# Kernel optimization log

Measured on AMD Instinct MI355X. Metric: run time of the kernel, lower is better.

## Reference

```python
import jax, jax.numpy as jnp
import numpy as np

B, S, D, H = 2, 2048, 1024, 16
HD = D // H  # 64

def setup_inputs() -> dict:
    key = jax.random.key(0)
    ks = jax.random.split(key, 11)
    s = 1.0 / np.sqrt(D)
    inp = {
        "q": jax.random.normal(ks[0], (B, S, D), jnp.float32),
        "k": jax.random.normal(ks[1], (B, S, D), jnp.float32),
        "v": jax.random.normal(ks[2], (B, S, D), jnp.float32),
        "Wq": jax.random.normal(ks[3], (D, D), jnp.float32) * s,
        "bq": jnp.zeros((D,), jnp.float32),
        "Wk": jax.random.normal(ks[4], (D, D), jnp.float32) * s,
        "bk": jnp.zeros((D,), jnp.float32),
        "Wv": jax.random.normal(ks[5], (D, D), jnp.float32) * s,
        "bv": jnp.zeros((D,), jnp.float32),
        "Wo": jax.random.normal(ks[6], (D, D), jnp.float32) * s,
        "bo": jnp.zeros((D,), jnp.float32),
    }
    return inp

def _split_heads(x):
    # [B,S,D] -> [B,H,S,HD]
    b = x.shape[0]
    return x.reshape(b, -1, H, HD).transpose(0, 2, 1, 3)

def reference(q, k, v, Wq, bq, Wk, bk, Wv, bv, Wo, bo):
    qh = _split_heads(q @ Wq.T + bq)
    kh = _split_heads(k @ Wk.T + bk)
    vh = _split_heads(v @ Wv.T + bv)
    scale = 1.0 / jnp.sqrt(jnp.asarray(HD, qh.dtype))
    scores = jnp.einsum("bhqd,bhkd->bhqk", qh, kh) * scale  # [B,H,S,S]
    atten = jax.nn.softmax(scores, axis=-1)  # dropout is eval-mode no-op
    ctx = jnp.einsum("bhqk,bhkd->bhqd", atten, vh)
    out = ctx.transpose(0, 2, 1, 3).reshape(q.shape[0], -1, D)
    return out @ Wo.T + bo, atten
```

## Files before the change

kernel.cpp:

```cpp
#include <hip/hip_runtime.h>
#include <cstdint>

#define B_ 2
#define S_ 2048
#define D_ 1024
#define H_ 16

typedef __bf16 bf16x8 __attribute__((ext_vector_type(8)));
typedef float  f32x4  __attribute__((ext_vector_type(4)));

__device__ __forceinline__ void g2l16(const void* g, void* l) {
  auto* gp = reinterpret_cast<const __attribute__((address_space(1))) uint32_t*>(
      reinterpret_cast<uintptr_t>(g));
  auto* lp = reinterpret_cast<__attribute__((address_space(3))) uint32_t*>(
      reinterpret_cast<uintptr_t>(l));
  __builtin_amdgcn_global_load_lds(gp, lp, 16, 0, 0);
}

__device__ __forceinline__ float exp2_hw(float x) {
#if __has_builtin(__builtin_amdgcn_exp2f)
  return __builtin_amdgcn_exp2f(x);
#else
  return __exp2f(x);
#endif
}

struct CvtArgs {
  const float* s[7];
  __bf16* d[7];
  int n[7];
};

__global__ __launch_bounds__(256) void k_cvt(CvtArgs a) {
  int t = blockIdx.y;
  long i = (long)blockIdx.x * blockDim.x + threadIdx.x;
  long base = i * 8;
  if (base >= a.n[t]) return;
  const float4* sp = (const float4*)(a.s[t] + base);
  float4 x = sp[0], y = sp[1];
  bf16x8 o;
  o[0] = (__bf16)x.x; o[1] = (__bf16)x.y; o[2] = (__bf16)x.z; o[3] = (__bf16)x.w;
  o[4] = (__bf16)y.x; o[5] = (__bf16)y.y; o[6] = (__bf16)y.z; o[7] = (__bf16)y.w;
  *(bf16x8*)(a.d[t] + base) = o;
}

__global__ __launch_bounds__(256, 3) void k_proj(
    const __bf16* __restrict__ Xq, const __bf16* __restrict__ Xk, const __bf16* __restrict__ Xv,
    const __bf16* __restrict__ Wq, const __bf16* __restrict__ Wk, const __bf16* __restrict__ Wv,
    const float* __restrict__ bq, const float* __restrict__ bk, const float* __restrict__ bv,
    __bf16* __restrict__ Oq, __bf16* __restrict__ Ok, __bf16* __restrict__ Ov)
{
  int z = blockIdx.z;
  const __bf16* X = (z == 0) ? Xq : (z == 1) ? Xk : Xv;
  const __bf16* W = (z == 0) ? Wq : (z == 1) ? Wk : Wv;
  const float* bias = (z == 0) ? bq : (z == 1) ? bk : bv;
  __bf16* O = (z == 0) ? Oq : (z == 1) ? Ok : Ov;
  float scale = (z == 0) ? 0.180336880111183f : 1.0f;

  __shared__ bf16x8 As[3][512];
  __shared__ bf16x8 Bs[3][512];

  int t = threadIdx.x, lane = t & 63, w = t >> 6;
  int l15 = lane & 15, l4 = lane >> 4;
  int wr = w >> 1, wc = w & 1;
  int m0 = blockIdx.y * 128, n0 = blockIdx.x * 128;

  int srow = t >> 2, sc = t & 3;
  int ldsoff = __builtin_amdgcn_readfirstlane(w * 1024);
  const __bf16* Xs = X + (size_t)(m0 + srow) * 1024 + sc * 8;
  const __bf16* Wsp = W + (size_t)(n0 + srow) * 1024 + sc * 8;

#define PSTAGE(buf, kt)                                                        \
  {                                                                            \
    _Pragma("unroll")                                                          \
    for (int i = 0; i < 2; ++i) {                                              \
      int lo = __builtin_amdgcn_readfirstlane(i * 4096 + ldsoff);              \
      g2l16(Xs + (size_t)i * 64 * 1024 + (kt) * 32, (char*)As[buf] + lo);      \
      g2l16(Wsp + (size_t)i * 64 * 1024 + (kt) * 32, (char*)Bs[buf] + lo);     \
    }                                                                          \
  }

  f32x4 acc[4][4] = {};

  PSTAGE(0, 0)
  PSTAGE(1, 1)
  asm volatile("s_waitcnt vmcnt(4)" ::: "memory");
  __builtin_amdgcn_s_barrier();
  __builtin_amdgcn_sched_barrier(0);

  int ring = 0;
  for (int kt = 0; kt < 32; ++kt) {
    int cur = ring;
    int rp2 = (ring == 0) ? 2 : ring - 1;
    if (kt + 2 < 32) PSTAGE(rp2, kt + 2)
    __builtin_amdgcn_sched_barrier(0);

    bf16x8 af[4], bfr[4];
#pragma unroll
    for (int i = 0; i < 4; ++i) af[i] = As[cur][(wr * 64 + i * 16 + l15) * 4 + l4];
#pragma unroll
    for (int j = 0; j < 4; ++j) bfr[j] = Bs[cur][(wc * 64 + j * 16 + l15) * 4 + l4];
#pragma unroll
    for (int i = 0; i < 4; ++i)
#pragma unroll
      for (int j = 0; j < 4; ++j)
        acc[i][j] = __builtin_amdgcn_mfma_f32_16x16x32_bf16(af[i], bfr[j], acc[i][j], 0, 0, 0);

    if (kt < 30) {
      asm volatile("s_waitcnt vmcnt(4)" ::: "memory");
      __builtin_amdgcn_s_barrier();
      __builtin_amdgcn_sched_barrier(0);
    } else if (kt == 30) {
      asm volatile("s_waitcnt vmcnt(0)" ::: "memory");
      __builtin_amdgcn_s_barrier();
      __builtin_amdgcn_sched_barrier(0);
    }
    ring = (ring == 2) ? 0 : ring + 1;
  }
#undef PSTAGE

#pragma unroll
  for (int j = 0; j < 4; ++j) {
    int col = n0 + wc * 64 + j * 16 + l15;
    float bv_ = bias[col];
    int h = col >> 6, hd = col & 63;
#pragma unroll
    for (int i = 0; i < 4; ++i) {
#pragma unroll
      for (int r = 0; r < 4; ++r) {
        int row = m0 + wr * 64 + i * 16 + l4 * 4 + r;
        int b = row >> 11, ss = row & 2047;
        float val = (acc[i][j][r] + bv_) * scale;
        O[(((size_t)b * H_ + h) * S_ + ss) * 64 + hd] = (__bf16)val;
      }
    }
  }
}

__global__ __launch_bounds__(256) void k_trans(const __bf16* __restrict__ Vh,
                                               __bf16* __restrict__ VhT)
{
  __shared__ __bf16 Tt[64][72];
  int bid = blockIdx.x;
  int bh = bid >> 5, st = bid & 31;
  int t = threadIdx.x;
  int sr = t >> 2, dc = (t & 3) * 16;
  const __bf16* src = Vh + (((size_t)bh * S_) + st * 64 + sr) * 64 + dc;
  *(bf16x8*)&Tt[sr][dc] = *(const bf16x8*)src;
  *(bf16x8*)&Tt[sr][dc + 8] = *(const bf16x8*)(src + 8);
  __syncthreads();
  int dr = t >> 2, s0 = (t & 3) * 16;
  bf16x8 o0, o1;
#pragma unroll
  for (int ii = 0; ii < 8; ++ii) { o0[ii] = Tt[s0 + ii][dr]; o1[ii] = Tt[s0 + 8 + ii][dr]; }
  __bf16* dst = VhT + ((size_t)bh * 64 + dr) * S_ + st * 64 + s0;
  *(bf16x8*)dst = o0;
  *(bf16x8*)(dst + 8) = o1;
}

__global__ __launch_bounds__(512, 4) void k_attn(
    const __bf16* __restrict__ Qh, const __bf16* __restrict__ Kh,
    const __bf16* __restrict__ VhT, float* __restrict__ atten,
    __bf16* __restrict__ ctxb)
{
  __shared__ bf16x8 KVl[3][1024];
  __shared__ bf16x8 Pl[8 * 176];

  int bid = blockIdx.x;
  int sb = (bid & 7) * 64 + (bid >> 3);
  int bh = sb >> 4, qt = sb & 15;
  int t = threadIdx.x, lane = t & 63, w = t >> 6;
  int l15 = lane & 15, l4 = lane >> 4;
  int q0 = qt * 128 + w * 16;

  const __bf16* Qp = Qh + ((size_t)bh * S_ + q0) * 64;
  bf16x8 qf0 = *(const bf16x8*)(Qp + (size_t)l15 * 64 + l4 * 8);
  bf16x8 qf1 = *(const bf16x8*)(Qp + (size_t)l15 * 64 + 32 + l4 * 8);

  int srow = t >> 3, sc8 = t & 7;
  int scs = sc8 ^ (srow & 7);
  int wbase = __builtin_amdgcn_readfirstlane(w * 1024);

  const __bf16* KpS = Kh + (size_t)bh * S_ * 64 + (size_t)srow * 64 + scs * 8;
  const __bf16* VpS = VhT + (size_t)bh * 64 * S_ + (size_t)srow * S_ + scs * 8;

  float l_part[4] = {0.f, 0.f, 0.f, 0.f};

#define ASTAGE(buf, kt)                                                        \
  {                                                                            \
    g2l16(KpS + (size_t)(kt) * 8192, (char*)KVl[buf] + wbase);                 \
    g2l16(KpS + (size_t)(kt) * 8192 + 4096, (char*)KVl[buf] + 8192 + wbase);   \
  }

  ASTAGE(0, 0)
  ASTAGE(1, 1)
  asm volatile("s_waitcnt vmcnt(2)" ::: "memory");
  __builtin_amdgcn_s_barrier();
  __builtin_amdgcn_sched_barrier(0);

  {
    int ring = 0;
    for (int kt = 0; kt < 16; ++kt) {
      int cur = ring;
      int rp2 = (ring == 0) ? 2 : ring - 1;
      if (kt + 2 < 16) ASTAGE(rp2, kt + 2)
      __builtin_amdgcn_sched_barrier(0);

#pragma unroll
      for (int t8 = 0; t8 < 8; ++t8) {
        int kr = t8 * 16 + l15;
        bf16x8 kf0 = KVl[cur][kr * 8 + ((l4) ^ (kr & 7))];
        bf16x8 kf1 = KVl[cur][kr * 8 + ((4 + l4) ^ (kr & 7))];
        f32x4 a_ = {0.f, 0.f, 0.f, 0.f};
        a_ = __builtin_amdgcn_mfma_f32_16x16x32_bf16(qf0, kf0, a_, 0, 0, 0);
        a_ = __builtin_amdgcn_mfma_f32_16x16x32_bf16(qf1, kf1, a_, 0, 0, 0);
#pragma unroll
        for (int r = 0; r < 4; ++r) l_part[r] += exp2_hw(a_[r]);
      }

      if (kt < 14) {
        asm volatile("s_waitcnt vmcnt(2)" ::: "memory");
        __builtin_amdgcn_s_barrier();
        __builtin_amdgcn_sched_barrier(0);
      } else if (kt == 14) {
        asm volatile("s_waitcnt vmcnt(0)" ::: "memory");
        __builtin_amdgcn_s_barrier();
        __builtin_amdgcn_sched_barrier(0);
      }
      ring = (ring == 2) ? 0 : ring + 1;
    }
  }
#undef ASTAGE

  float inv_l[4];
#pragma unroll
  for (int r = 0; r < 4; ++r) {
    float l = l_part[r];
    l += __shfl_xor(l, 1);
    l += __shfl_xor(l, 2);
    l += __shfl_xor(l, 4);
    l += __shfl_xor(l, 8);
    inv_l[r] = 1.0f / l;
  }

  __builtin_amdgcn_s_barrier();
  __builtin_amdgcn_sched_barrier(0);

  f32x4 ctx[4] = {};
  float* aRow = atten + ((size_t)bh * S_ + q0) * S_;
  __bf16* PlW = (__bf16*)(Pl + w * 176);

#define BSTAGE(buf, kt)                                                        \
  {                                                                            \
    g2l16(KpS + (size_t)(kt) * 4096, (char*)KVl[buf] + wbase);                 \
    g2l16(VpS + (size_t)(kt) * 64, (char*)KVl[buf] + 8192 + wbase);            \
  }

  BSTAGE(0, 0)
  BSTAGE(1, 1)
  asm volatile("s_waitcnt vmcnt(2)" ::: "memory");
  __builtin_amdgcn_s_barrier();
  __builtin_amdgcn_sched_barrier(0);

  {
    int ring = 0;
    for (int kt = 0; kt < 32; ++kt) {
      int cur = ring;
      int rp2 = (ring == 0) ? 2 : ring - 1;
      if (kt + 2 < 32) BSTAGE(rp2, kt + 2)
      __builtin_amdgcn_sched_barrier(0);

      f32x4 sc[4];
#pragma unroll
      for (int t8 = 0; t8 < 4; ++t8) {
        int kr = t8 * 16 + l15;
        bf16x8 kf0 = KVl[cur][kr * 8 + ((l4) ^ (kr & 7))];
        bf16x8 kf1 = KVl[cur][kr * 8 + ((4 + l4) ^ (kr & 7))];
        f32x4 a_ = {0.f, 0.f, 0.f, 0.f};
        a_ = __builtin_amdgcn_mfma_f32_16x16x32_bf16(qf0, kf0, a_, 0, 0, 0);
        a_ = __builtin_amdgcn_mfma_f32_16x16x32_bf16(qf1, kf1, a_, 0, 0, 0);
        sc[t8] = a_;
      }

#pragma unroll
      for (int t8 = 0; t8 < 4; ++t8) {
#pragma unroll
        for (int r = 0; r < 4; ++r) {
          float p = exp2_hw(sc[t8][r]) * inv_l[r];
          aRow[(size_t)(l4 * 4 + r) * S_ + kt * 64 + t8 * 16 + l15] = p;
          PlW[(l4 * 4 + r) * 88 + t8 * 16 + l15] = (__bf16)p;
        }
      }

#pragma unroll
      for (int kc = 0; kc < 2; ++kc) {
        bf16x8 pa = Pl[w * 176 + l15 * 11 + kc * 4 + l4];
#pragma unroll
        for (int dt = 0; dt < 4; ++dt) {
          int vr = dt * 16 + l15;
          bf16x8 vf = KVl[cur][512 + vr * 8 + ((kc * 4 + l4) ^ (vr & 7))];
          ctx[dt] = __builtin_amdgcn_mfma_f32_16x16x32_bf16(pa, vf, ctx[dt], 0, 0, 0);
        }
      }

      if (kt < 31) {
        asm volatile("s_waitcnt vmcnt(18)" ::: "memory");
        __builtin_amdgcn_s_barrier();
        __builtin_amdgcn_sched_barrier(0);
      }
      ring = (ring == 2) ? 0 : ring + 1;
    }
  }
#undef BSTAGE

  int b = bh >> 4, h = bh & 15;
#pragma unroll
  for (int dt = 0; dt < 4; ++dt) {
#pragma unroll
    for (int r = 0; r < 4; ++r) {
      size_t row = (size_t)b * S_ + q0 + l4 * 4 + r;
      ctxb[row * D_ + h * 64 + dt * 16 + l15] = (__bf16)ctx[dt][r];
    }
  }
}

__global__ __launch_bounds__(256, 3) void k_out(
    const __bf16* __restrict__ X, const __bf16* __restrict__ W,
    const float* __restrict__ bias, float* __restrict__ O)
{
  __shared__ bf16x8 As[3][512];
  __shared__ bf16x8 Bs[3][512];

  int t = threadIdx.x, lane = t & 63, w = t >> 6;
  int l15 = lane & 15, l4 = lane >> 4;
  int wr = w >> 1, wc = w & 1;
  int m0 = blockIdx.y * 128, n0 = blockIdx.x * 128;

  int srow = t >> 2, sc = t & 3;
  int ldsoff = __builtin_amdgcn_readfirstlane(w * 1024);
  const __bf16* Xs = X + (size_t)(m0 + srow) * 1024 + sc * 8;
  const __bf16* Wsp = W + (size_t)(n0 + srow) * 1024 + sc * 8;

#define PSTAGE(buf, kt)                                                        \
  {                                                                            \
    _Pragma("unroll")                                                          \
    for (int i = 0; i < 2; ++i) {                                              \
      int lo = __builtin_amdgcn_readfirstlane(i * 4096 + ldsoff);              \
      g2l16(Xs + (size_t)i * 64 * 1024 + (kt) * 32, (char*)As[buf] + lo);      \
      g2l16(Wsp + (size_t)i * 64 * 1024 + (kt) * 32, (char*)Bs[buf] + lo);     \
    }                                                                          \
  }

  f32x4 acc[4][4] = {};

  PSTAGE(0, 0)
  PSTAGE(1, 1)
  asm volatile("s_waitcnt vmcnt(4)" ::: "memory");
  __builtin_amdgcn_s_barrier();
  __builtin_amdgcn_sched_barrier(0);

  int ring = 0;
  for (int kt = 0; kt < 32; ++kt) {
    int cur = ring;
    int rp2 = (ring == 0) ? 2 : ring - 1;
    if (kt + 2 < 32) PSTAGE(rp2, kt + 2)
    __builtin_amdgcn_sched_barrier(0);

    bf16x8 af[4], bfr[4];
#pragma unroll
    for (int i = 0; i < 4; ++i) af[i] = As[cur][(wr * 64 + i * 16 + l15) * 4 + l4];
#pragma unroll
    for (int j = 0; j < 4; ++j) bfr[j] = Bs[cur][(wc * 64 + j * 16 + l15) * 4 + l4];
#pragma unroll
    for (int i = 0; i < 4; ++i)
#pragma unroll
      for (int j = 0; j < 4; ++j)
        acc[i][j] = __builtin_amdgcn_mfma_f32_16x16x32_bf16(af[i], bfr[j], acc[i][j], 0, 0, 0);

    if (kt < 30) {
      asm volatile("s_waitcnt vmcnt(4)" ::: "memory");
      __builtin_amdgcn_s_barrier();
      __builtin_amdgcn_sched_barrier(0);
    } else if (kt == 30) {
      asm volatile("s_waitcnt vmcnt(0)" ::: "memory");
      __builtin_amdgcn_s_barrier();
      __builtin_amdgcn_sched_barrier(0);
    }
    ring = (ring == 2) ? 0 : ring + 1;
  }
#undef PSTAGE

#pragma unroll
  for (int j = 0; j < 4; ++j) {
    int col = n0 + wc * 64 + j * 16 + l15;
    float bv_ = bias[col];
#pragma unroll
    for (int i = 0; i < 4; ++i) {
#pragma unroll
      for (int r = 0; r < 4; ++r) {
        int row = m0 + wr * 64 + i * 16 + l4 * 4 + r;
        O[(size_t)row * 1024 + col] = acc[i][j][r] + bv_;
      }
    }
  }
}

extern "C" void kernel_launch(void* const* d_in, const int* in_sizes, int n_in,
                              void* d_out, int out_size, void* d_ws, size_t ws_size,
                              hipStream_t stream)
{
  const float* q  = (const float*)d_in[0];
  const float* k  = (const float*)d_in[1];
  const float* v  = (const float*)d_in[2];
  const float* Wq = (const float*)d_in[3];
  const float* bq = (const float*)d_in[4];
  const float* Wk = (const float*)d_in[5];
  const float* bk = (const float*)d_in[6];
  const float* Wv = (const float*)d_in[7];
  const float* bv = (const float*)d_in[8];
  const float* Wo = (const float*)d_in[9];
  const float* bo = (const float*)d_in[10];

  const size_t NBSD = (size_t)B_ * S_ * D_;
  const size_t NDD  = (size_t)D_ * D_;

  float* out = (float*)d_out;
  float* atten = out + NBSD;

  if (ws_size < 2 * (NBSD * 4 + NDD * 4 + NBSD * 4)) return;

  __bf16* ws = (__bf16*)d_ws;
  __bf16* qb  = ws;
  __bf16* kb  = ws + NBSD;
  __bf16* vb  = ws + 2 * NBSD;
  __bf16* Wqb = ws + 3 * NBSD;
  __bf16* Wkb = Wqb + NDD;
  __bf16* Wvb = Wkb + NDD;
  __bf16* Wob = Wvb + NDD;
  __bf16* Qh  = Wob + NDD;
  __bf16* Kh  = Qh + NBSD;
  __bf16* Vh  = Kh + NBSD;
  __bf16* VhT = Vh + NBSD;
  __bf16* ctxb = qb;

  CvtArgs ca;
  ca.s[0] = q;  ca.d[0] = qb;  ca.n[0] = (int)NBSD;
  ca.s[1] = k;  ca.d[1] = kb;  ca.n[1] = (int)NBSD;
  ca.s[2] = v;  ca.d[2] = vb;  ca.n[2] = (int)NBSD;
  ca.s[3] = Wq; ca.d[3] = Wqb; ca.n[3] = (int)NDD;
  ca.s[4] = Wk; ca.d[4] = Wkb; ca.n[4] = (int)NDD;
  ca.s[5] = Wv; ca.d[5] = Wvb; ca.n[5] = (int)NDD;
  ca.s[6] = Wo; ca.d[6] = Wob; ca.n[6] = (int)NDD;

  k_cvt<<<dim3(2048, 7), 256, 0, stream>>>(ca);
  k_proj<<<dim3(8, 32, 3), 256, 0, stream>>>(qb, kb, vb, Wqb, Wkb, Wvb,
                                             bq, bk, bv, Qh, Kh, Vh);
  k_trans<<<dim3(1024), 256, 0, stream>>>(Vh, VhT);
  k_attn<<<dim3(512), 512, 0, stream>>>(Qh, Kh, VhT, atten, ctxb);
  k_out<<<dim3(8, 32), 256, 0, stream>>>(ctxb, Wob, bo, out);
}
```

Baseline: 261.5 us.

## Fuse activation fp32→bf16 conversion and V transpose into projection GEMM

The projection kernel now loads fp32 activations directly into registers, converts them to bf16 and writes them to LDS, so the separate conversion pass over q/k/v is dropped and k_cvt only converts weights. The V projection epilogue stages its tile through LDS and writes the transposed layout directly, which removes the k_trans kernel and its extra global round trip. The cost is that A-tile loads become register-staged with double buffering instead of async global-to-LDS copies, and the GEMM main loop now reads twice the bytes for the activation operand.

New measurement: 256.6 us. Within noise of the previous version (-1.8%).

```diff
diff --git a/kernel.cpp b/kernel.cpp
--- a/kernel.cpp
+++ b/kernel.cpp
@@ -7,6 +7,7 @@
 #define H_ 16
 
 typedef __bf16 bf16x8 __attribute__((ext_vector_type(8)));
+typedef __bf16 bf16x4 __attribute__((ext_vector_type(4)));
 typedef float  f32x4  __attribute__((ext_vector_type(4)));
 
 __device__ __forceinline__ void g2l16(const void* g, void* l) {
@@ -26,16 +27,13 @@
 }
 
 struct CvtArgs {
-  const float* s[7];
-  __bf16* d[7];
-  int n[7];
+  const float* s[4];
+  __bf16* d[4];
 };
 
 __global__ __launch_bounds__(256) void k_cvt(CvtArgs a) {
   int t = blockIdx.y;
-  long i = (long)blockIdx.x * blockDim.x + threadIdx.x;
-  long base = i * 8;
-  if (base >= a.n[t]) return;
+  long base = ((long)blockIdx.x * blockDim.x + threadIdx.x) * 8;
   const float4* sp = (const float4*)(a.s[t] + base);
   float4 x = sp[0], y = sp[1];
   bf16x8 o;
@@ -45,117 +43,161 @@
 }
 
 __global__ __launch_bounds__(256, 3) void k_proj(
-    const __bf16* __restrict__ Xq, const __bf16* __restrict__ Xk, const __bf16* __restrict__ Xv,
+    const float* __restrict__ Xq, const float* __restrict__ Xk, const float* __restrict__ Xv,
     const __bf16* __restrict__ Wq, const __bf16* __restrict__ Wk, const __bf16* __restrict__ Wv,
     const float* __restrict__ bq, const float* __restrict__ bk, const float* __restrict__ bv,
-    __bf16* __restrict__ Oq, __bf16* __restrict__ Ok, __bf16* __restrict__ Ov)
+    __bf16* __restrict__ Oq, __bf16* __restrict__ Ok, __bf16* __restrict__ OvT)
 {
   int z = blockIdx.z;
-  const __bf16* X = (z == 0) ? Xq : (z == 1) ? Xk : Xv;
+  const float* X = (z == 0) ? Xq : (z == 1) ? Xk : Xv;
   const __bf16* W = (z == 0) ? Wq : (z == 1) ? Wk : Wv;
   const float* bias = (z == 0) ? bq : (z == 1) ? bk : bv;
-  __bf16* O = (z == 0) ? Oq : (z == 1) ? Ok : Ov;
   float scale = (z == 0) ? 0.180336880111183f : 1.0f;
 
-  __shared__ bf16x8 As[3][512];
-  __shared__ bf16x8 Bs[3][512];
+  __shared__ __align__(16) char smem[40960];
+  bf16x8 (*As)[512] = (bf16x8(*)[512])smem;
+  bf16x8 (*Bs)[512] = (bf16x8(*)[512])(smem + 16384);
 
   int t = threadIdx.x, lane = t & 63, w = t >> 6;
   int l15 = lane & 15, l4 = lane >> 4;
   int wr = w >> 1, wc = w & 1;
   int m0 = blockIdx.y * 128, n0 = blockIdx.x * 128;
 
+  int arow = t >> 1, ac2 = (t & 1) * 2;
+  const float* Xs = X + (size_t)(m0 + arow) * 1024 + (t & 1) * 16;
   int srow = t >> 2, sc = t & 3;
+  const __bf16* Wsp = W + (size_t)(n0 + srow) * 1024 + sc * 8;
   int ldsoff = __builtin_amdgcn_readfirstlane(w * 1024);
-  const __bf16* Xs = X + (size_t)(m0 + srow) * 1024 + sc * 8;
-  const __bf16* Wsp = W + (size_t)(n0 + srow) * 1024 + sc * 8;
-
-#define PSTAGE(buf, kt)                                                        \
+
+  float4 a0, a1, a2, a3;
+
+#define ALOAD(kt)                                                              \
+  {                                                                            \
+    const float4* ap = (const float4*)(Xs + (size_t)(kt) * 32);                \
+    a0 = ap[0]; a1 = ap[1]; a2 = ap[2]; a3 = ap[3];                            \
+  }
+#define AWRITE(buf)                                                            \
+  {                                                                            \
+    bf16x8 lo, hi;                                                             \
+    lo[0] = (__bf16)a0.x; lo[1] = (__bf16)a0.y; lo[2] = (__bf16)a0.z;          \
+    lo[3] = (__bf16)a0.w; lo[4] = (__bf16)a1.x; lo[5] = (__bf16)a1.y;          \
+    lo[6] = (__bf16)a1.z; lo[7] = (__bf16)a1.w;                                \
+    hi[0] = (__bf16)a2.x; hi[1] = (__bf16)a2.y; hi[2] = (__bf16)a2.z;          \
+    hi[3] = (__bf16)a2.w; hi[4] = (__bf16)a3.x; hi[5] = (__bf16)a3.y;          \
+    hi[6] = (__bf16)a3.z; hi[7] = (__bf16)a3.w;                                \
+    As[buf][arow * 4 + ac2] = lo;                                              \
+    As[buf][arow * 4 + ac2 + 1] = hi;                                          \
+  }
+#define BSTG(buf, kt)                                                          \
   {                                                                            \
     _Pragma("unroll")                                                          \
     for (int i = 0; i < 2; ++i) {                                              \
-      int lo = __builtin_amdgcn_readfirstlane(i * 4096 + ldsoff);              \
-      g2l16(Xs + (size_t)i * 64 * 1024 + (kt) * 32, (char*)As[buf] + lo);      \
-      g2l16(Wsp + (size_t)i * 64 * 1024 + (kt) * 32, (char*)Bs[buf] + lo);     \
+      int lo_ = __builtin_amdgcn_readfirstlane(i * 4096 + ldsoff);             \
+      g2l16(Wsp + (size_t)i * 64 * 1024 + (kt) * 32, (char*)Bs[buf] + lo_);    \
     }                                                                          \
   }
 
   f32x4 acc[4][4] = {};
 
-  PSTAGE(0, 0)
-  PSTAGE(1, 1)
-  asm volatile("s_waitcnt vmcnt(4)" ::: "memory");
+  BSTG(0, 0)
+  ALOAD(0)
+  BSTG(1, 1)
+  asm volatile("s_waitcnt vmcnt(2)" ::: "memory");
+  AWRITE(0)
+  ALOAD(1)
+  asm volatile("s_waitcnt lgkmcnt(0)" ::: "memory");
   __builtin_amdgcn_s_barrier();
   __builtin_amdgcn_sched_barrier(0);
 
-  int ring = 0;
+  int bring = 0;
   for (int kt = 0; kt < 32; ++kt) {
-    int cur = ring;
-    int rp2 = (ring == 0) ? 2 : ring - 1;
-    if (kt + 2 < 32) PSTAGE(rp2, kt + 2)
+    int bcur = bring;
+    int bp2 = (bring >= 1) ? bring - 1 : 2;
+    int acur = kt & 1, anxt = acur ^ 1;
+    if (kt + 2 < 32) BSTG(bp2, kt + 2)
     __builtin_amdgcn_sched_barrier(0);
 
     bf16x8 af[4], bfr[4];
 #pragma unroll
-    for (int i = 0; i < 4; ++i) af[i] = As[cur][(wr * 64 + i * 16 + l15) * 4 + l4];
-#pragma unroll
-    for (int j = 0; j < 4; ++j) bfr[j] = Bs[cur][(wc * 64 + j * 16 + l15) * 4 + l4];
+    for (int i = 0; i < 4; ++i) af[i] = As[acur][(wr * 64 + i * 16 + l15) * 4 + l4];
+#pragma unroll
+    for (int j = 0; j < 4; ++j) bfr[j] = Bs[bcur][(wc * 64 + j * 16 + l15) * 4 + l4];
 #pragma unroll
     for (int i = 0; i < 4; ++i)
 #pragma unroll
       for (int j = 0; j < 4; ++j)
         acc[i][j] = __builtin_amdgcn_mfma_f32_16x16x32_bf16(af[i], bfr[j], acc[i][j], 0, 0, 0);
-
-    if (kt < 30) {
-      asm volatile("s_waitcnt vmcnt(4)" ::: "memory");
+    __builtin_amdgcn_sched_barrier(0);
+
+    if (kt + 1 < 32) {
+      if (kt + 2 < 32) {
+        asm volatile("s_waitcnt vmcnt(2)" ::: "memory");
+      } else {
+        asm volatile("s_waitcnt vmcnt(0)" ::: "memory");
+      }
+      AWRITE(anxt)
+      if (kt + 2 < 32) ALOAD(kt + 2)
+      asm volatile("s_waitcnt lgkmcnt(0)" ::: "memory");
       __builtin_amdgcn_s_barrier();
       __builtin_amdgcn_sched_barrier(0);
-    } else if (kt == 30) {
-      asm volatile("s_waitcnt vmcnt(0)" ::: "memory");
-      __builtin_amdgcn_s_barrier();
-      __builtin_amdgcn_sched_barrier(0);
-    }
-    ring = (ring == 2) ? 0 : ring + 1;
-  }
-#undef PSTAGE
-
-#pragma unroll
-  for (int j = 0; j < 4; ++j) {
-    int col = n0 + wc * 64 + j * 16 + l15;
-    float bv_ = bias[col];
-    int h = col >> 6, hd = col & 63;
-#pragma unroll
-    for (int i = 0; i < 4; ++i) {
-#pragma unroll
-      for (int r = 0; r < 4; ++r) {
-        int row = m0 + wr * 64 + i * 16 + l4 * 4 + r;
-        int b = row >> 11, ss = row & 2047;
-        float val = (acc[i][j][r] + bv_) * scale;
-        O[(((size_t)b * H_ + h) * S_ + ss) * 64 + hd] = (__bf16)val;
-      }
-    }
-  }
-}
-
-__global__ __launch_bounds__(256) void k_trans(const __bf16* __restrict__ Vh,
-                                               __bf16* __restrict__ VhT)
-{
-  __shared__ __bf16 Tt[64][72];
-  int bid = blockIdx.x;
-  int bh = bid >> 5, st = bid & 31;
-  int t = threadIdx.x;
-  int sr = t >> 2, dc = (t & 3) * 16;
-  const __bf16* src = Vh + (((size_t)bh * S_) + st * 64 + sr) * 64 + dc;
-  *(bf16x8*)&Tt[sr][dc] = *(const bf16x8*)src;
-  *(bf16x8*)&Tt[sr][dc + 8] = *(const bf16x8*)(src + 8);
-  __syncthreads();
-  int dr = t >> 2, s0 = (t & 3) * 16;
-  bf16x8 o0, o1;
-#pragma unroll
-  for (int ii = 0; ii < 8; ++ii) { o0[ii] = Tt[s0 + ii][dr]; o1[ii] = Tt[s0 + 8 + ii][dr]; }
-  __bf16* dst = VhT + ((size_t)bh * 64 + dr) * S_ + st * 64 + s0;
-  *(bf16x8*)dst = o0;
-  *(bf16x8*)(dst + 8) = o1;
+    }
+    bring = (bring == 2) ? 0 : bring + 1;
+  }
+#undef ALOAD
+#undef AWRITE
+#undef BSTG
+
+  if (z == 2) {
+    __syncthreads();
+    __bf16* Tt = (__bf16*)smem;
+    const int LDT = 136;
+    int b = m0 >> 11, ss0 = m0 & 2047;
+#pragma unroll
+    for (int p = 0; p < 2; ++p) {
+      if (wc == p) {
+#pragma unroll
+        for (int j = 0; j < 4; ++j) {
+          float bv_ = bias[n0 + p * 64 + j * 16 + l15];
+#pragma unroll
+          for (int i = 0; i < 4; ++i) {
+            bf16x4 pv;
+#pragma unroll
+            for (int r = 0; r < 4; ++r) pv[r] = (__bf16)(acc[i][j][r] + bv_);
+            *(bf16x4*)&Tt[(j * 16 + l15) * LDT + wr * 64 + i * 16 + l4 * 4] = pv;
+          }
+        }
+      }
+      __syncthreads();
+      int h = (n0 >> 6) + p;
+      __bf16* dst = OvT + ((size_t)(b * H_ + h) * 64) * S_ + ss0;
+#pragma unroll
+      for (int it = 0; it < 4; ++it) {
+        int nl = it * 16 + (t >> 4);
+        int mc = (t & 15) * 8;
+        bf16x8 vv = *(bf16x8*)&Tt[nl * LDT + mc];
+        *(bf16x8*)(dst + (size_t)nl * S_ + mc) = vv;
+      }
+      __syncthreads();
+    }
+  } else {
+    __bf16* O = (z == 0) ? Oq : Ok;
+#pragma unroll
+    for (int j = 0; j < 4; ++j) {
+      int col = n0 + wc * 64 + j * 16 + l15;
+      float bv_ = bias[col];
+      int h = col >> 6, hd = col & 63;
+#pragma unroll
+      for (int i = 0; i < 4; ++i) {
+#pragma unroll
+        for (int r = 0; r < 4; ++r) {
+          int row = m0 + wr * 64 + i * 16 + l4 * 4 + r;
+          int b = row >> 11, ss = row & 2047;
+          float val = (acc[i][j][r] + bv_) * scale;
+          O[(((size_t)b * H_ + h) * S_ + ss) * 64 + hd] = (__bf16)val;
+        }
+      }
+    }
+  }
 }
 
 __global__ __launch_bounds__(512, 4) void k_attn(
@@ -427,35 +469,27 @@
   float* out = (float*)d_out;
   float* atten = out + NBSD;
 
-  if (ws_size < 2 * (NBSD * 4 + NDD * 4 + NBSD * 4)) return;
+  if (ws_size < (4 * NDD + 4 * NBSD) * 2) return;
 
   __bf16* ws = (__bf16*)d_ws;
-  __bf16* qb  = ws;
-  __bf16* kb  = ws + NBSD;
-  __bf16* vb  = ws + 2 * NBSD;
-  __bf16* Wqb = ws + 3 * NBSD;
+  __bf16* Wqb = ws;
   __bf16* Wkb = Wqb + NDD;
   __bf16* Wvb = Wkb + NDD;
   __bf16* Wob = Wvb + NDD;
   __bf16* Qh  = Wob + NDD;
   __bf16* Kh  = Qh + NBSD;
-  __bf16* Vh  = Kh + NBSD;
-  __bf16* VhT = Vh + NBSD;
-  __bf16* ctxb = qb;
+  __bf16* VhT = Kh + NBSD;
+  __bf16* ctxb = VhT + NBSD;
 
   CvtArgs ca;
-  ca.s[0] = q;  ca.d[0] = qb;  ca.n[0] = (int)NBSD;
-  ca.s[1] = k;  ca.d[1] = kb;  ca.n[1] = (int)NBSD;
-  ca.s[2] = v;  ca.d[2] = vb;  ca.n[2] = (int)NBSD;
-  ca.s[3] = Wq; ca.d[3] = Wqb; ca.n[3] = (int)NDD;
-  ca.s[4] = Wk; ca.d[4] = Wkb; ca.n[4] = (int)NDD;
-  ca.s[5] = Wv; ca.d[5] = Wvb; ca.n[5] = (int)NDD;
-  ca.s[6] = Wo; ca.d[6] = Wob; ca.n[6] = (int)NDD;
-
-  k_cvt<<<dim3(2048, 7), 256, 0, stream>>>(ca);
-  k_proj<<<dim3(8, 32, 3), 256, 0, stream>>>(qb, kb, vb, Wqb, Wkb, Wvb,
-                                             bq, bk, bv, Qh, Kh, Vh);
-  k_trans<<<dim3(1024), 256, 0, stream>>>(Vh, VhT);
+  ca.s[0] = Wq; ca.d[0] = Wqb;
+  ca.s[1] = Wk; ca.d[1] = Wkb;
+  ca.s[2] = Wv; ca.d[2] = Wvb;
+  ca.s[3] = Wo; ca.d[3] = Wob;
+
+  k_cvt<<<dim3(512, 4), 256, 0, stream>>>(ca);
+  k_proj<<<dim3(8, 32, 3), 256, 0, stream>>>(q, k, v, Wqb, Wkb, Wvb,
+                                             bq, bk, bv, Qh, Kh, VhT);
   k_attn<<<dim3(512), 512, 0, stream>>>(Qh, Kh, VhT, atten, ctxb);
   k_out<<<dim3(8, 32), 256, 0, stream>>>(ctxb, Wob, bo, out);
 }
```
